# Kernel tuning notes

Measured on AMD Instinct MI355X. Metric: run time of the kernel, lower is better.

The kernel has to match this reference:

```python
import jax, jax.numpy as jnp
import numpy as np

N_NODES = 100000
N_EDGES = 1600000
IN_DIM = 256
OUT_DIM = 128


def setup_inputs() -> dict:
    key = jax.random.key(0)
    k1, k2, k3, k4, k5 = jax.random.split(key, 5)
    inputs = jax.random.normal(k1, (N_NODES, IN_DIM), dtype=jnp.float32)
    # xavier_uniform with relu gain, as in the torch init
    gain = float(np.sqrt(2.0))
    limit = gain * float(np.sqrt(6.0 / (IN_DIM + OUT_DIM)))
    W = jax.random.uniform(k2, (IN_DIM, OUT_DIM), dtype=jnp.float32,
                           minval=-limit, maxval=limit)
    edge_src = jax.random.randint(k3, (N_EDGES,), 0, N_NODES, dtype=jnp.int32)
    edge_dst = jax.random.randint(k4, (N_EDGES,), 0, N_NODES, dtype=jnp.int32)
    edge_val = jax.random.uniform(k5, (N_EDGES,), dtype=jnp.float32)
    return {"inputs": inputs, "W": W, "edge_src": edge_src,
            "edge_dst": edge_dst, "edge_val": edge_val}


def reference(inputs, W, edge_src, edge_dst, edge_val):
    # x = inputs @ W  (dense GEMM)
    h = inputs @ W                                  # [N, OUT_DIM]
    # adj @ h  as SpMM over COO edges: out[d] += val * h[s]
    msg = edge_val[:, None] * h[edge_src]           # [E, OUT_DIM]
    agg = jax.ops.segment_sum(msg, edge_dst, num_segments=N_NODES)
    # act = ReLU, fused with SpMM output
    return jax.nn.relu(agg)
```

## Files before the change

### kernel.cpp

```cpp
#include <hip/hip_runtime.h>
#include <hip/hip_bf16.h>

#define N_NODES 100000
#define N_EDGES 1600000
#define IN_DIM  256
#define OUT_DIM 128

#define GEMM_ROWS   32
#define GEMM_BLOCKS (N_NODES / GEMM_ROWS)

#define NBUCK   196
#define BSHIFT  9
#define BCAP    10240
#define BSTRIDE 16
#define EPB     2048
#define BIN_BLOCKS ((N_EDGES + EPB - 1) / EPB)
#define TOTAL_BLOCKS (GEMM_BLOCKS + BIN_BLOCKS)

typedef __attribute__((ext_vector_type(8))) short bf16x8;
typedef __attribute__((ext_vector_type(4))) float f32x4;

__device__ __forceinline__ ushort f2bf(float f) {
    union { float f; unsigned u; } v; v.f = f;
    unsigned r = v.u + 0x7FFF + ((v.u >> 16) & 1);
    return (ushort)(r >> 16);
}
__device__ __forceinline__ float bflo(unsigned u) {
    union { unsigned u; float f; } v; v.u = u << 16; return v.f;
}
__device__ __forceinline__ float bfhi(unsigned u) {
    union { unsigned u; float f; } v; v.u = u & 0xFFFF0000u; return v.f;
}

__global__ __launch_bounds__(256) void pack_w(const float* __restrict__ W,
                                              ushort* __restrict__ Wp,
                                              int* __restrict__ bcur) {
    const int t = blockIdx.x * 256 + threadIdx.x;
    if (blockIdx.x == 0) {
        for (int i = threadIdx.x; i < NBUCK * BSTRIDE; i += 256) bcur[i] = 0;
    }
    if (t >= 4096) return;
    const int kk = t >> 9, n = (t >> 6) & 7, l = t & 63;
    const int kbase = kk * 32 + (l >> 4) * 8;
    const int col   = n * 16 + (l & 15);
    ushort* o = Wp + (size_t)t * 8;
#pragma unroll
    for (int j = 0; j < 8; ++j)
        o[j] = f2bf(W[(size_t)(kbase + j) * OUT_DIM + col]);
}

__global__ __launch_bounds__(256, 5) void gemm_coarse(const float* __restrict__ X,
                                                      const bf16x8* __restrict__ Bp,
                                                      ushort* __restrict__ H,
                                                      const int* __restrict__ esrc,
                                                      const int* __restrict__ edst,
                                                      const float* __restrict__ eval,
                                                      int* __restrict__ bcur,
                                                      int2* __restrict__ binned) {
    __shared__ char smem[22656];

    const int tid  = threadIdx.x;
    const int lane = tid & 63;
    const int wv   = tid >> 6;
    const int bid  = blockIdx.x;

    const bool is_coarse = ((bid % 5) == 4) || (bid == TOTAL_BLOCKS - 1);

    if (is_coarse) {
        const int blk = (bid == TOTAL_BLOCKS - 1) ? (BIN_BLOCKS - 1) : (bid / 5);
        int*   cnt   = (int*)smem;
        int*   lbase = (int*)smem + 256;
        int*   sbase = (int*)smem + 512;
        int*   cur   = (int*)smem + 768;
        int2*  lrec  = (int2*)(smem + 4096);
        unsigned char* lbid = (unsigned char*)smem + 20480;

        const int cb  = blk * EPB;
        const int lim = (N_EDGES - cb < EPB) ? (N_EDGES - cb) : EPB;

        if (tid < NBUCK) cnt[tid] = 0;
        __syncthreads();
        for (int i = tid; i < lim; i += 256)
            atomicAdd(&cnt[edst[cb + i] >> BSHIFT], 1);
        __syncthreads();

        {
            __shared__ int wsum[4];
            const int v = (tid < NBUCK) ? cnt[tid] : 0;
            int sv = v;
#pragma unroll
            for (int d = 1; d < 64; d <<= 1) {
                const int t = __shfl_up(sv, d, 64);
                if (lane >= d) sv += t;
            }
            if (lane == 63) wsum[wv] = sv;
            __syncthreads();
            int wx = 0;
#pragma unroll
            for (int w = 0; w < 4; ++w) if (w < wv) wx += wsum[w];
            if (tid < NBUCK) {
                const int ex = wx + sv - v;
                lbase[tid] = ex;
                cur[tid]   = ex;
                sbase[tid] = v ? atomicAdd(&bcur[tid * BSTRIDE], v) : 0;
            }
        }
        __syncthreads();

        for (int i = tid; i < lim; i += 256) {
            const int d = edst[cb + i];
            const int b = d >> BSHIFT;
            const int pos = atomicAdd(&cur[b], 1);
            int2 rec;
            rec.x = esrc[cb + i] | ((d & 511) << 20);
            rec.y = __float_as_int(eval[cb + i]);
            lrec[pos] = rec;
            lbid[pos] = (unsigned char)b;
        }
        __syncthreads();

        for (int i = tid; i < lim; i += 256) {
            const int b   = lbid[i];
            const int off = sbase[b] + (i - lbase[b]);
            if (off < BCAP)
                binned[(size_t)b * BCAP + off] = lrec[i];
        }
        return;
    }

    const int gidx = bid - bid / 5;
    ushort* xt = (ushort*)smem;
    const int row0 = gidx * GEMM_ROWS;
    const int wid  = wv;

#pragma unroll 4
    for (int it = 0; it < 8; ++it) {
        const int tr = it * 4 + (tid >> 6);
        const int tc = (tid & 63) * 4;
        const float4 v = *reinterpret_cast<const float4*>(
            X + (size_t)(row0 + tr) * IN_DIM + tc);
        ushort4 b4;
        b4.x = f2bf(v.x); b4.y = f2bf(v.y); b4.z = f2bf(v.z); b4.w = f2bf(v.w);
        const int byte = (tr * 512 + tc * 2) ^ ((tr & 7) << 4);
        *reinterpret_cast<ushort4*>((char*)xt + byte) = b4;
    }

    bf16x8 Bfr[8][2];
#pragma unroll
    for (int kk = 0; kk < 8; ++kk)
#pragma unroll
        for (int n = 0; n < 2; ++n)
            Bfr[kk][n] = Bp[(size_t)(kk * 8 + wid * 2 + n) * 64 + lane];

    __syncthreads();

    const int rlo  = lane & 15;
    const int kseg = lane >> 4;
    const int rl0  = rlo;
    const int rl1  = rlo + 16;
    const int rxor = (rlo & 7) << 4;

    f32x4 acc[2][2] = {};

#pragma unroll
    for (int kk = 0; kk < 8; ++kk) {
        const int cb2 = (kk * 64 + kseg * 16) ^ rxor;
        const bf16x8 A0 = *reinterpret_cast<const bf16x8*>((const char*)xt + rl0 * 512 + cb2);
        const bf16x8 A1 = *reinterpret_cast<const bf16x8*>((const char*)xt + rl1 * 512 + cb2);
#pragma unroll
        for (int n = 0; n < 2; ++n) {
            acc[0][n] = __builtin_amdgcn_mfma_f32_16x16x32_bf16(A0, Bfr[kk][n], acc[0][n], 0, 0, 0);
            acc[1][n] = __builtin_amdgcn_mfma_f32_16x16x32_bf16(A1, Bfr[kk][n], acc[1][n], 0, 0, 0);
        }
    }

#pragma unroll
    for (int i = 0; i < 2; ++i)
#pragma unroll
        for (int r = 0; r < 4; ++r)
#pragma unroll
            for (int n = 0; n < 2; ++n)
                H[(size_t)(row0 + i * 16 + kseg * 4 + r) * OUT_DIM
                  + wid * 32 + n * 16 + rlo] = f2bf(acc[i][n][r]);
}

__global__ __launch_bounds__(1024) void bin_fine(const int* __restrict__ bcur,
                                                 const int2* __restrict__ binned,
                                                 int* __restrict__ offsets,
                                                 int2* __restrict__ recs) {
    __shared__ int nh[512];
    __shared__ int cur[512];
    __shared__ int ws[4];
    __shared__ int wsB[4];
    __shared__ int base_out_s;
    const int b   = blockIdx.x;
    const int tid = threadIdx.x, lane = tid & 63, wid = tid >> 6;
    const int node0 = b << BSHIFT;
    int nn = N_NODES - node0; if (nn > 512) nn = 512;
    int size = bcur[b * BSTRIDE]; if (size > BCAP) size = BCAP;
    const int2* in = binned + (size_t)b * BCAP;

    if (tid < 256) {
        const int v = (tid < NBUCK) ? bcur[tid * BSTRIDE] : 0;
        int sv = v;
#pragma unroll
        for (int d = 1; d < 64; d <<= 1) {
            const int t = __shfl_up(sv, d, 64);
            if (lane >= d) sv += t;
        }
        if (lane == 63) wsB[wid] = sv;
        __syncthreads();
        int wx = 0;
#pragma unroll
        for (int w = 0; w < 4; ++w) if (w < wid) wx += wsB[w];
        if (tid == b) base_out_s = wx + sv - v;
    } else {
        __syncthreads();
    }

    if (tid < 512) nh[tid] = 0;
    __syncthreads();
    const int base_out = base_out_s;
    for (int k = tid; k < size; k += 1024)
        atomicAdd(&nh[(in[k].x >> 20) & 511], 1);
    __syncthreads();

    int a0 = 0, ts = 0, sv = 0;
    if (tid < 256) {
        a0 = nh[2 * tid];
        const int a1 = nh[2 * tid + 1];
        ts = a0 + a1;
        sv = ts;
#pragma unroll
        for (int d = 1; d < 64; d <<= 1) {
            const int t = __shfl_up(sv, d, 64);
            if (lane >= d) sv += t;
        }
        if (lane == 63) ws[wid] = sv;
    }
    __syncthreads();
    if (tid < 256) {
        int wx = 0;
#pragma unroll
        for (int w = 0; w < 4; ++w) if (w < wid) wx += ws[w];
        const int ex = wx + sv - ts;
        cur[2 * tid]     = base_out + ex;
        cur[2 * tid + 1] = base_out + ex + a0;
        if (2 * tid < nn)     offsets[node0 + 2 * tid]     = base_out + ex;
        if (2 * tid + 1 < nn) offsets[node0 + 2 * tid + 1] = base_out + ex + a0;
    }
    if (b == 0 && tid == 0) offsets[N_NODES] = N_EDGES;
    __syncthreads();

    for (int k = tid; k < size; k += 1024) {
        const int2 r = in[k];
        const int pos = atomicAdd(&cur[(r.x >> 20) & 511], 1);
        int2 o; o.x = r.x & 0xFFFFF; o.y = r.y;
        recs[pos] = o;
    }
}

__global__ __launch_bounds__(256) void spmm_pull(const ushort* __restrict__ H,
                                                 const int* __restrict__ offsets,
                                                 const int2* __restrict__ recs,
                                                 float* __restrict__ out) {
    const int tid   = threadIdx.x;
    const int lane  = tid & 63;
    const int g     = lane >> 4;
    const int c     = lane & 15;
    const int gwave = blockIdx.x * 4 + (tid >> 6);
    const int node  = gwave * 4 + g;
    if (node >= N_NODES) return;

    const int beg = offsets[node];
    const int end = offsets[node + 1];

    float a0 = 0.f, a1 = 0.f, a2 = 0.f, a3 = 0.f;
    float a4 = 0.f, a5 = 0.f, a6 = 0.f, a7 = 0.f;

#define ACC(h, v)  {                                                      \
        a0 = fmaf(v, bflo(h.x), a0);  a1 = fmaf(v, bfhi(h.x), a1);        \
        a2 = fmaf(v, bflo(h.y), a2);  a3 = fmaf(v, bfhi(h.y), a3);        \
        a4 = fmaf(v, bflo(h.z), a4);  a5 = fmaf(v, bfhi(h.z), a5);        \
        a6 = fmaf(v, bflo(h.w), a6);  a7 = fmaf(v, bfhi(h.w), a7); }

    int e = beg;
    for (; e + 7 < end; e += 8) {
        const int2 r0 = recs[e + 0], r1 = recs[e + 1];
        const int2 r2 = recs[e + 2], r3 = recs[e + 3];
        const int2 r4 = recs[e + 4], r5 = recs[e + 5];
        const int2 r6 = recs[e + 6], r7 = recs[e + 7];
        const uint4 h0 = *((const uint4*)(H + (size_t)r0.x * OUT_DIM) + c);
        const uint4 h1 = *((const uint4*)(H + (size_t)r1.x * OUT_DIM) + c);
        const uint4 h2 = *((const uint4*)(H + (size_t)r2.x * OUT_DIM) + c);
        const uint4 h3 = *((const uint4*)(H + (size_t)r3.x * OUT_DIM) + c);
        const uint4 h4 = *((const uint4*)(H + (size_t)r4.x * OUT_DIM) + c);
        const uint4 h5 = *((const uint4*)(H + (size_t)r5.x * OUT_DIM) + c);
        const uint4 h6 = *((const uint4*)(H + (size_t)r6.x * OUT_DIM) + c);
        const uint4 h7 = *((const uint4*)(H + (size_t)r7.x * OUT_DIM) + c);
        ACC(h0, __int_as_float(r0.y));  ACC(h1, __int_as_float(r1.y));
        ACC(h2, __int_as_float(r2.y));  ACC(h3, __int_as_float(r3.y));
        ACC(h4, __int_as_float(r4.y));  ACC(h5, __int_as_float(r5.y));
        ACC(h6, __int_as_float(r6.y));  ACC(h7, __int_as_float(r7.y));
    }
    for (; e + 1 < end; e += 2) {
        const int2 r0 = recs[e + 0], r1 = recs[e + 1];
        const uint4 h0 = *((const uint4*)(H + (size_t)r0.x * OUT_DIM) + c);
        const uint4 h1 = *((const uint4*)(H + (size_t)r1.x * OUT_DIM) + c);
        ACC(h0, __int_as_float(r0.y));  ACC(h1, __int_as_float(r1.y));
    }
    if (e < end) {
        const int2 r0 = recs[e];
        const uint4 h0 = *((const uint4*)(H + (size_t)r0.x * OUT_DIM) + c);
        ACC(h0, __int_as_float(r0.y));
    }
#undef ACC

    float* op = out + (size_t)node * OUT_DIM + c * 8;
    float4 o0, o1;
    o0.x = fmaxf(a0, 0.f); o0.y = fmaxf(a1, 0.f);
    o0.z = fmaxf(a2, 0.f); o0.w = fmaxf(a3, 0.f);
    o1.x = fmaxf(a4, 0.f); o1.y = fmaxf(a5, 0.f);
    o1.z = fmaxf(a6, 0.f); o1.w = fmaxf(a7, 0.f);
    *reinterpret_cast<float4*>(op)     = o0;
    *reinterpret_cast<float4*>(op + 4) = o1;
}

extern "C" void kernel_launch(void* const* d_in, const int* in_sizes, int n_in,
                              void* d_out, int out_size, void* d_ws, size_t ws_size,
                              hipStream_t stream) {
    const float* X    = (const float*)d_in[0];
    const float* W    = (const float*)d_in[1];
    const int*   esrc = (const int*)d_in[2];
    const int*   edst = (const int*)d_in[3];
    const float* eval = (const float*)d_in[4];
    float*       out  = (float*)d_out;

    char* ws = (char*)d_ws;
    ushort* Hb     = (ushort*)ws;  ws += (size_t)N_NODES * OUT_DIM * sizeof(ushort);
    ushort* Wp     = (ushort*)ws;  ws += (size_t)4096 * 8 * sizeof(ushort);
    int*    offsets= (int*)ws;     ws += (((size_t)(N_NODES + 1) * 4 + 127) & ~(size_t)127);
    int*    bcur   = (int*)ws;     ws += (size_t)NBUCK * BSTRIDE * 4;
    int2*   binned = (int2*)ws;    ws += (size_t)NBUCK * BCAP * sizeof(int2);
    int2*   recs   = (int2*)ws;

    pack_w<<<16, 256, 0, stream>>>(W, Wp, bcur);
    gemm_coarse<<<TOTAL_BLOCKS, 256, 0, stream>>>(X, (const bf16x8*)Wp, Hb,
                                                  esrc, edst, eval, bcur, binned);

    bin_fine<<<NBUCK, 1024, 0, stream>>>(bcur, binned, offsets, recs);

    spmm_pull<<<(N_NODES + 15) / 16, 256, 0, stream>>>(Hb, offsets, recs, out);
}
```

Measured before the change: 123.0 us.

## Fuse fine binning and SpMM pull into a single per-bucket kernel

Merges the fine-binning kernel and the SpMM pull kernel into one. Each of the 196 bucket blocks first scatters its edges into CSR order, then gathers and reduces its own 512 destination nodes using the shared-memory cursors and counts as row bounds. This removes the global offsets array, its writes and reads, and one kernel launch. The cost is that the gather phase now runs on only 196 blocks of 1024 threads, fewer than the number of CUs, with each 16-lane group walking 8 nodes one after another, so latency hiding and load balance for the gather-bound SpMM may suffer.

```diff
diff --git a/kernel.cpp b/kernel.cpp
--- a/kernel.cpp
+++ b/kernel.cpp
@@ -184,10 +184,11 @@
                   + wid * 32 + n * 16 + rlo] = f2bf(acc[i][n][r]);
 }
 
-__global__ __launch_bounds__(1024) void bin_fine(const int* __restrict__ bcur,
+__global__ __launch_bounds__(1024) void bin_pull(const int* __restrict__ bcur,
                                                  const int2* __restrict__ binned,
-                                                 int* __restrict__ offsets,
-                                                 int2* __restrict__ recs) {
+                                                 int2* __restrict__ recs,
+                                                 const ushort* __restrict__ H,
+                                                 float* __restrict__ out) {
     __shared__ int nh[512];
     __shared__ int cur[512];
     __shared__ int ws[4];
@@ -246,10 +247,7 @@
         const int ex = wx + sv - ts;
         cur[2 * tid]     = base_out + ex;
         cur[2 * tid + 1] = base_out + ex + a0;
-        if (2 * tid < nn)     offsets[node0 + 2 * tid]     = base_out + ex;
-        if (2 * tid + 1 < nn) offsets[node0 + 2 * tid + 1] = base_out + ex + a0;
-    }
-    if (b == 0 && tid == 0) offsets[N_NODES] = N_EDGES;
+    }
     __syncthreads();
 
     for (int k = tid; k < size; k += 1024) {
@@ -258,72 +256,67 @@
         int2 o; o.x = r.x & 0xFFFFF; o.y = r.y;
         recs[pos] = o;
     }
-}
-
-__global__ __launch_bounds__(256) void spmm_pull(const ushort* __restrict__ H,
-                                                 const int* __restrict__ offsets,
-                                                 const int2* __restrict__ recs,
-                                                 float* __restrict__ out) {
-    const int tid   = threadIdx.x;
-    const int lane  = tid & 63;
-    const int g     = lane >> 4;
-    const int c     = lane & 15;
-    const int gwave = blockIdx.x * 4 + (tid >> 6);
-    const int node  = gwave * 4 + g;
-    if (node >= N_NODES) return;
-
-    const int beg = offsets[node];
-    const int end = offsets[node + 1];
-
-    float a0 = 0.f, a1 = 0.f, a2 = 0.f, a3 = 0.f;
-    float a4 = 0.f, a5 = 0.f, a6 = 0.f, a7 = 0.f;
+    __syncthreads();
+
+    const int grp = tid >> 4;
+    const int c   = tid & 15;
 
 #define ACC(h, v)  {                                                      \
-        a0 = fmaf(v, bflo(h.x), a0);  a1 = fmaf(v, bfhi(h.x), a1);        \
-        a2 = fmaf(v, bflo(h.y), a2);  a3 = fmaf(v, bfhi(h.y), a3);        \
-        a4 = fmaf(v, bflo(h.z), a4);  a5 = fmaf(v, bfhi(h.z), a5);        \
-        a6 = fmaf(v, bflo(h.w), a6);  a7 = fmaf(v, bfhi(h.w), a7); }
-
-    int e = beg;
-    for (; e + 7 < end; e += 8) {
-        const int2 r0 = recs[e + 0], r1 = recs[e + 1];
-        const int2 r2 = recs[e + 2], r3 = recs[e + 3];
-        const int2 r4 = recs[e + 4], r5 = recs[e + 5];
-        const int2 r6 = recs[e + 6], r7 = recs[e + 7];
-        const uint4 h0 = *((const uint4*)(H + (size_t)r0.x * OUT_DIM) + c);
-        const uint4 h1 = *((const uint4*)(H + (size_t)r1.x * OUT_DIM) + c);
-        const uint4 h2 = *((const uint4*)(H + (size_t)r2.x * OUT_DIM) + c);
-        const uint4 h3 = *((const uint4*)(H + (size_t)r3.x * OUT_DIM) + c);
-        const uint4 h4 = *((const uint4*)(H + (size_t)r4.x * OUT_DIM) + c);
-        const uint4 h5 = *((const uint4*)(H + (size_t)r5.x * OUT_DIM) + c);
-        const uint4 h6 = *((const uint4*)(H + (size_t)r6.x * OUT_DIM) + c);
-        const uint4 h7 = *((const uint4*)(H + (size_t)r7.x * OUT_DIM) + c);
-        ACC(h0, __int_as_float(r0.y));  ACC(h1, __int_as_float(r1.y));
-        ACC(h2, __int_as_float(r2.y));  ACC(h3, __int_as_float(r3.y));
-        ACC(h4, __int_as_float(r4.y));  ACC(h5, __int_as_float(r5.y));
-        ACC(h6, __int_as_float(r6.y));  ACC(h7, __int_as_float(r7.y));
-    }
-    for (; e + 1 < end; e += 2) {
-        const int2 r0 = recs[e + 0], r1 = recs[e + 1];
-        const uint4 h0 = *((const uint4*)(H + (size_t)r0.x * OUT_DIM) + c);
-        const uint4 h1 = *((const uint4*)(H + (size_t)r1.x * OUT_DIM) + c);
-        ACC(h0, __int_as_float(r0.y));  ACC(h1, __int_as_float(r1.y));
-    }
-    if (e < end) {
-        const int2 r0 = recs[e];
-        const uint4 h0 = *((const uint4*)(H + (size_t)r0.x * OUT_DIM) + c);
-        ACC(h0, __int_as_float(r0.y));
+        p0 = fmaf(v, bflo(h.x), p0);  p1 = fmaf(v, bfhi(h.x), p1);        \
+        p2 = fmaf(v, bflo(h.y), p2);  p3 = fmaf(v, bfhi(h.y), p3);        \
+        p4 = fmaf(v, bflo(h.z), p4);  p5 = fmaf(v, bfhi(h.z), p5);        \
+        p6 = fmaf(v, bflo(h.w), p6);  p7 = fmaf(v, bfhi(h.w), p7); }
+
+    for (int j = 0; j < 8; ++j) {
+        const int ln = grp * 8 + j;
+        if (ln >= nn) break;
+        const int end = cur[ln];
+        const int beg = end - nh[ln];
+
+        float p0 = 0.f, p1 = 0.f, p2 = 0.f, p3 = 0.f;
+        float p4 = 0.f, p5 = 0.f, p6 = 0.f, p7 = 0.f;
+
+        int e = beg;
+        for (; e + 7 < end; e += 8) {
+            const int2 r0 = recs[e + 0], r1 = recs[e + 1];
+            const int2 r2 = recs[e + 2], r3 = recs[e + 3];
+            const int2 r4 = recs[e + 4], r5 = recs[e + 5];
+            const int2 r6 = recs[e + 6], r7 = recs[e + 7];
+            const uint4 h0 = *((const uint4*)(H + (size_t)r0.x * OUT_DIM) + c);
+            const uint4 h1 = *((const uint4*)(H + (size_t)r1.x * OUT_DIM) + c);
+            const uint4 h2 = *((const uint4*)(H + (size_t)r2.x * OUT_DIM) + c);
+            const uint4 h3 = *((const uint4*)(H + (size_t)r3.x * OUT_DIM) + c);
+            const uint4 h4 = *((const uint4*)(H + (size_t)r4.x * OUT_DIM) + c);
+            const uint4 h5 = *((const uint4*)(H + (size_t)r5.x * OUT_DIM) + c);
+            const uint4 h6 = *((const uint4*)(H + (size_t)r6.x * OUT_DIM) + c);
+            const uint4 h7 = *((const uint4*)(H + (size_t)r7.x * OUT_DIM) + c);
+            ACC(h0, __int_as_float(r0.y));  ACC(h1, __int_as_float(r1.y));
+            ACC(h2, __int_as_float(r2.y));  ACC(h3, __int_as_float(r3.y));
+            ACC(h4, __int_as_float(r4.y));  ACC(h5, __int_as_float(r5.y));
+            ACC(h6, __int_as_float(r6.y));  ACC(h7, __int_as_float(r7.y));
+        }
+        for (; e + 1 < end; e += 2) {
+            const int2 r0 = recs[e + 0], r1 = recs[e + 1];
+            const uint4 h0 = *((const uint4*)(H + (size_t)r0.x * OUT_DIM) + c);
+            const uint4 h1 = *((const uint4*)(H + (size_t)r1.x * OUT_DIM) + c);
+            ACC(h0, __int_as_float(r0.y));  ACC(h1, __int_as_float(r1.y));
+        }
+        if (e < end) {
+            const int2 r0 = recs[e];
+            const uint4 h0 = *((const uint4*)(H + (size_t)r0.x * OUT_DIM) + c);
+            ACC(h0, __int_as_float(r0.y));
+        }
+
+        float* op = out + (size_t)(node0 + ln) * OUT_DIM + c * 8;
+        float4 o0, o1;
+        o0.x = fmaxf(p0, 0.f); o0.y = fmaxf(p1, 0.f);
+        o0.z = fmaxf(p2, 0.f); o0.w = fmaxf(p3, 0.f);
+        o1.x = fmaxf(p4, 0.f); o1.y = fmaxf(p5, 0.f);
+        o1.z = fmaxf(p6, 0.f); o1.w = fmaxf(p7, 0.f);
+        *reinterpret_cast<float4*>(op)     = o0;
+        *reinterpret_cast<float4*>(op + 4) = o1;
     }
 #undef ACC
-
-    float* op = out + (size_t)node * OUT_DIM + c * 8;
-    float4 o0, o1;
-    o0.x = fmaxf(a0, 0.f); o0.y = fmaxf(a1, 0.f);
-    o0.z = fmaxf(a2, 0.f); o0.w = fmaxf(a3, 0.f);
-    o1.x = fmaxf(a4, 0.f); o1.y = fmaxf(a5, 0.f);
-    o1.z = fmaxf(a6, 0.f); o1.w = fmaxf(a7, 0.f);
-    *reinterpret_cast<float4*>(op)     = o0;
-    *reinterpret_cast<float4*>(op + 4) = o1;
 }
 
 extern "C" void kernel_launch(void* const* d_in, const int* in_sizes, int n_in,
@@ -339,7 +332,6 @@
     char* ws = (char*)d_ws;
     ushort* Hb     = (ushort*)ws;  ws += (size_t)N_NODES * OUT_DIM * sizeof(ushort);
     ushort* Wp     = (ushort*)ws;  ws += (size_t)4096 * 8 * sizeof(ushort);
-    int*    offsets= (int*)ws;     ws += (((size_t)(N_NODES + 1) * 4 + 127) & ~(size_t)127);
     int*    bcur   = (int*)ws;     ws += (size_t)NBUCK * BSTRIDE * 4;
     int2*   binned = (int2*)ws;    ws += (size_t)NBUCK * BCAP * sizeof(int2);
     int2*   recs   = (int2*)ws;
@@ -348,7 +340,5 @@
     gemm_coarse<<<TOTAL_BLOCKS, 256, 0, stream>>>(X, (const bf16x8*)Wp, Hb,
                                                   esrc, edst, eval, bcur, binned);
 
-    bin_fine<<<NBUCK, 1024, 0, stream>>>(bcur, binned, offsets, recs);
-
-    spmm_pull<<<(N_NODES + 15) / 16, 256, 0, stream>>>(Hb, offsets, recs, out);
-}
+    bin_pull<<<NBUCK, 1024, 0, stream>>>(bcur, binned, recs, Hb, out);
+}
```

After: 122.5 us. No clear change (-0.4%).
